# Performance work log

Hardware: AMD Instinct MI355X
Metric: run time of the kernel (lower is better)

## Reference

```python
import jax, jax.numpy as jnp
import numpy as np

B, D, T, BINS = 8, 768, 16384, 1024

def setup_inputs() -> dict:
    key = jax.random.key(0)
    k1, k2, k3, k4 = jax.random.split(key, 4)
    ssl_content = jax.random.normal(k1, (B, D, T), dtype=jnp.float32)
    conv_w = jax.random.normal(k2, (D, D, 2), dtype=jnp.float32) * 0.02  # Conv1d(768,768,k=2,s=2) weight [out,in,k]
    conv_b = jax.random.normal(k3, (D,), dtype=jnp.float32) * 0.02
    codebook = jax.random.normal(k4, (BINS, D), dtype=jnp.float32)
    return {"ssl_content": ssl_content, "conv_w": conv_w, "conv_b": conv_b, "codebook": codebook}

def reference(ssl_content, conv_w, conv_b, codebook):
    # ssl_proj: Conv1d(D, D, kernel_size=2, stride=2), no padding
    ssl = jax.lax.conv_general_dilated(
        ssl_content, conv_w, window_strides=(2,), padding='VALID',
        dimension_numbers=('NCH', 'OIH', 'NCH')) + conv_b[None, :, None]  # [B, D, T//2]
    x = jnp.transpose(ssl, (0, 2, 1))            # b d n -> b n d : [B, T', D]
    b, tq, d = x.shape
    flat = x.reshape(-1, d)                      # [B*T', D]
    # Euclidean codebook search: argmin_k ||flat - codebook[k]||^2
    d2 = (jnp.sum(flat * flat, axis=-1, keepdims=True)
          - 2.0 * (flat @ codebook.T)
          + jnp.sum(codebook * codebook, axis=-1))  # [B*T', BINS]
    codes = jnp.argmin(d2, axis=-1).reshape(b, tq)  # n_q=1 -> indices for quantizer 0: [B, T']
    prompt = codes[0][None, :]                   # codes[0,0].unsqueeze(0) -> [1, T']
    return prompt
```

## Files before the change

### kernel.cpp

```cpp
#include <hip/hip_runtime.h>

#define D    768
#define T    16384
#define TQ   8192
#define BINS 1024
#define K1   1536
#define NKA  (K1 / 32)
#define NKS  (D / 32)
#define FRAG 1024

#define NFRAG_W  ((D / 16) * NKA)
#define NFRAG_CB ((BINS / 16) * NKS)
#define NB_PACKB ((NFRAG_W + NFRAG_CB) / 4)
#define NB_PACKA (NKA * (TQ / 128))
#define NB_CNORM (BINS / 4)

typedef _Float16 f16;
typedef _Float16 h8 __attribute__((ext_vector_type(8)));
typedef float    f32x4 __attribute__((ext_vector_type(4)));


__device__ __forceinline__ void gl_lds16(const void* g, void* l) {
    __builtin_amdgcn_global_load_lds(
        (const __attribute__((address_space(1))) void*)g,
        (__attribute__((address_space(3))) void*)l, 16, 0, 0);
}

__global__ __launch_bounds__(256) void prep_kernel(
    const float* __restrict__ ssl, const float* __restrict__ W,
    const float* __restrict__ cb,
    f16* __restrict__ Whi, f16* __restrict__ Wlo,
    f16* __restrict__ CBhi, f16* __restrict__ CBlo,
    f16* __restrict__ Ahi, f16* __restrict__ Alo,
    float* __restrict__ cnorm)
{
    int b = blockIdx.x;
    int wid = threadIdx.x >> 6, lane = threadIdx.x & 63;

    if (b < NB_PACKB) {
        int fid = b * 4 + wid;
        const float* src; f16* hi; f16* lo; int K, nk, fidl;
        if (fid < NFRAG_W) { src = W;  hi = Whi;  lo = Wlo;  K = K1; nk = NKA; fidl = fid; }
        else               { src = cb; hi = CBhi; lo = CBlo; K = D;  nk = NKS; fidl = fid - NFRAG_W; }
        int r16 = fidl / nk, kblk = fidl - r16 * nk;
        int row = r16 * 16 + (lane & 15);
        int k0  = kblk * 32 + 8 * (lane >> 4);
        const float* s = src + (size_t)row * K + k0;
        float4 v0 = *(const float4*)s;
        float4 v1 = *(const float4*)(s + 4);
        float vv[8] = {v0.x, v0.y, v0.z, v0.w, v1.x, v1.y, v1.z, v1.w};
        h8 vh, vl;
        #pragma unroll
        for (int j = 0; j < 8; ++j) {
            f16 h = (f16)vv[j];
            vh[j] = h;
            vl[j] = (f16)((vv[j] - (float)h) * 2048.f);
        }
        size_t off = ((size_t)fidl * 64 + lane) * 8;
        *(h8*)&hi[off] = vh;
        *(h8*)&lo[off] = vl;
    } else if (b < NB_PACKB + NB_PACKA) {
        int idx = b - NB_PACKB;
        int kblk = idx % NKA, yb = idx / NKA;
        int l15 = lane & 15, lk = lane >> 4;
        #pragma unroll
        for (int q = 0; q < 2; ++q) {
            int tblk = yb * 8 + wid * 2 + q;
            int tp = tblk * 16 + l15;
            int i0 = kblk * 16 + 4 * lk;
            float vv[8];
            #pragma unroll
            for (int ii = 0; ii < 4; ++ii) {
                float2 v = *(const float2*)&ssl[(size_t)(i0 + ii) * T + 2 * tp];
                vv[2 * ii]     = v.x;
                vv[2 * ii + 1] = v.y;
            }
            h8 vh, vl;
            #pragma unroll
            for (int j = 0; j < 8; ++j) {
                f16 h = (f16)vv[j];
                vh[j] = h;
                vl[j] = (f16)((vv[j] - (float)h) * 2048.f);
            }
            size_t off = ((size_t)(tblk * NKA + kblk) * 64 + lane) * 8;
            *(h8*)&Ahi[off] = vh;
            *(h8*)&Alo[off] = vl;
        }
    } else {
        int bin = (b - NB_PACKB - NB_PACKA) * 4 + wid;
        const float* row = cb + (size_t)bin * D;
        float s = 0.f;
        for (int k = lane; k < D; k += 64) { float v = row[k]; s += v * v; }
        #pragma unroll
        for (int off = 32; off > 0; off >>= 1) s += __shfl_down(s, off);
        if (lane == 0) cnorm[bin] = s;
    }
}

__global__ __launch_bounds__(256, 2) void conv_mfma_kernel(
    const f16* __restrict__ Ah, const f16* __restrict__ Al,
    const f16* __restrict__ Bh, const f16* __restrict__ Bl,
    const float* __restrict__ bias,
    f16* __restrict__ Xhi, f16* __restrict__ Xlo)
{
    __shared__ __align__(16) char smem[65536];
    int tid = threadIdx.x, lane = tid & 63, wid = tid >> 6;
    int wm = wid >> 1, wn = wid & 1;
    int l15 = lane & 15, lk = lane >> 4;

    int orig = blockIdx.y * 6 + blockIdx.x;
    int swz  = (orig & 7) * 48 + (orig >> 3);
    int bx = swz % 6, by = swz / 6;

    int mb = by * 128, nb = bx * 128;
    int mb16 = mb >> 4, nb16 = nb >> 4;

    const f16* gsrc; int blk16;
    if      (wid == 0) { gsrc = Ah; blk16 = mb16; }
    else if (wid == 1) { gsrc = Al; blk16 = mb16; }
    else if (wid == 2) { gsrc = Bh; blk16 = nb16; }
    else               { gsrc = Bl; blk16 = nb16; }
    const char* gw = (const char*)gsrc + (size_t)blk16 * NKA * FRAG + lane * 16;
    char* lw0 = smem + wid * 8192;
    char* lw1 = smem + 32768 + wid * 8192;

    const f32x4 zero4 = {0.f, 0.f, 0.f, 0.f};
    f32x4 acc[4][4], acc2[4][4];
    #pragma unroll
    for (int i = 0; i < 4; ++i)
        #pragma unroll
        for (int j = 0; j < 4; ++j) { acc[i][j] = zero4; acc2[i][j] = zero4; }

    #pragma unroll
    for (int f = 0; f < 8; ++f)
        gl_lds16(gw + (size_t)(f * NKA) * FRAG, lw0 + f * FRAG);
    __syncthreads();

    int cur = 0;
    for (int kblk = 0; kblk < NKA; ++kblk) {
        if (kblk + 1 < NKA) {
            char* lwn = cur ? lw0 : lw1;
            #pragma unroll
            for (int f = 0; f < 8; ++f)
                gl_lds16(gw + (size_t)(f * NKA + kblk + 1) * FRAG, lwn + f * FRAG);
        }
        const char* base = smem + cur * 32768;
        h8 ah[4], al[4];
        #pragma unroll
        for (int mf = 0; mf < 4; ++mf) {
            int fo = (wm * 4 + mf) * FRAG + lane * 16;
            ah[mf] = *(const h8*)(base + fo);
            al[mf] = *(const h8*)(base + 8192 + fo);
        }
        #pragma unroll
        for (int nf = 0; nf < 4; ++nf) {
            int fo = (wn * 4 + nf) * FRAG + lane * 16;
            h8 bh = *(const h8*)(base + 16384 + fo);
            h8 bl = *(const h8*)(base + 24576 + fo);
            #pragma unroll
            for (int mf = 0; mf < 4; ++mf) {
                acc [mf][nf] = __builtin_amdgcn_mfma_f32_16x16x32_f16(ah[mf], bh, acc [mf][nf], 0, 0, 0);
                acc2[mf][nf] = __builtin_amdgcn_mfma_f32_16x16x32_f16(ah[mf], bl, acc2[mf][nf], 0, 0, 0);
                acc2[mf][nf] = __builtin_amdgcn_mfma_f32_16x16x32_f16(al[mf], bh, acc2[mf][nf], 0, 0, 0);
            }
        }
        __syncthreads();
        cur ^= 1;
    }

    float* sb = (float*)smem;
    float bv[4];
    #pragma unroll
    for (int nf = 0; nf < 4; ++nf) bv[nf] = bias[nb + wn * 64 + nf * 16 + l15];
    #pragma unroll
    for (int s = 0; s < 4; ++s) {
        __syncthreads();
        if (wm == (s >> 1)) {
            #pragma unroll
            for (int mh = 0; mh < 2; ++mh) {
                int mf = (s & 1) * 2 + mh;
                int srow = mh * 16 + lk * 4;
                #pragma unroll
                for (int nf = 0; nf < 4; ++nf) {
                    int scol = wn * 64 + nf * 16 + l15;
                    #pragma unroll
                    for (int r = 0; r < 4; ++r)
                        sb[(srow + r) * 132 + scol] =
                            acc[mf][nf][r] + acc2[mf][nf][r] * 4.8828125e-4f + bv[nf];
                }
            }
        }
        __syncthreads();
        #pragma unroll
        for (int h = 0; h < 2; ++h) {
            int f = wid * 2 + h;
            int tl = f & 1, dbl = f >> 1;
            int srow = tl * 16 + l15;
            int sd   = dbl * 32 + 8 * lk;
            float vv[8];
            #pragma unroll
            for (int j = 0; j < 8; ++j) vv[j] = sb[srow * 132 + sd + j];
            h8 vh, vl;
            #pragma unroll
            for (int j = 0; j < 8; ++j) {
                f16 hh = (f16)vv[j];
                vh[j] = hh;
                vl[j] = (f16)((vv[j] - (float)hh) * 2048.f);
            }
            int tblk_g = mb16 + s * 2 + tl;
            int dblk_g = (nb >> 5) + dbl;
            size_t off = ((size_t)(tblk_g * NKS + dblk_g) * 64 + lane) * 8;
            *(h8*)&Xhi[off] = vh;
            *(h8*)&Xlo[off] = vl;
        }
    }
}

__global__ __launch_bounds__(256, 2) void score_mfma_kernel(
    const f16* __restrict__ Ah, const f16* __restrict__ Al,
    const f16* __restrict__ Bh, const f16* __restrict__ Bl,
    const float* __restrict__ cnorm,
    float* __restrict__ pval, int* __restrict__ pidx)
{
    __shared__ __align__(16) char smem[65536];
    int tid = threadIdx.x, lane = tid & 63, wid = tid >> 6;
    int wm = wid >> 1, wn = wid & 1;
    int l15 = lane & 15, lk = lane >> 4;

    int orig = blockIdx.y * 8 + blockIdx.x;
    int swz  = (orig & 7) * 64 + (orig >> 3);
    int bx = swz & 7, by = swz >> 3;

    int mb = by * 128, nb = bx * 128;
    int mb16 = mb >> 4, nb16 = nb >> 4;

    const f16* gsrc; int blk16;
    if      (wid == 0) { gsrc = Ah; blk16 = mb16; }
    else if (wid == 1) { gsrc = Al; blk16 = mb16; }
    else if (wid == 2) { gsrc = Bh; blk16 = nb16; }
    else               { gsrc = Bl; blk16 = nb16; }
    const char* gw = (const char*)gsrc + (size_t)blk16 * NKS * FRAG + lane * 16;
    char* lw0 = smem + wid * 8192;
    char* lw1 = smem + 32768 + wid * 8192;

    const f32x4 zero4 = {0.f, 0.f, 0.f, 0.f};
    f32x4 acc[4][4], acc2[4][4];
    #pragma unroll
    for (int i = 0; i < 4; ++i)
        #pragma unroll
        for (int j = 0; j < 4; ++j) { acc[i][j] = zero4; acc2[i][j] = zero4; }

    #pragma unroll
    for (int f = 0; f < 8; ++f)
        gl_lds16(gw + (size_t)(f * NKS) * FRAG, lw0 + f * FRAG);
    __syncthreads();

    int cur = 0;
    for (int kblk = 0; kblk < NKS; ++kblk) {
        if (kblk + 1 < NKS) {
            char* lwn = cur ? lw0 : lw1;
            #pragma unroll
            for (int f = 0; f < 8; ++f)
                gl_lds16(gw + (size_t)(f * NKS + kblk + 1) * FRAG, lwn + f * FRAG);
        }
        const char* base = smem + cur * 32768;
        h8 ah[4], al[4];
        #pragma unroll
        for (int mf = 0; mf < 4; ++mf) {
            int fo = (wm * 4 + mf) * FRAG + lane * 16;
            ah[mf] = *(const h8*)(base + fo);
            al[mf] = *(const h8*)(base + 8192 + fo);
        }
        #pragma unroll
        for (int nf = 0; nf < 4; ++nf) {
            int fo = (wn * 4 + nf) * FRAG + lane * 16;
            h8 bh = *(const h8*)(base + 16384 + fo);
            h8 bl = *(const h8*)(base + 24576 + fo);
            #pragma unroll
            for (int mf = 0; mf < 4; ++mf) {
                acc [mf][nf] = __builtin_amdgcn_mfma_f32_16x16x32_f16(ah[mf], bh, acc [mf][nf], 0, 0, 0);
                acc2[mf][nf] = __builtin_amdgcn_mfma_f32_16x16x32_f16(ah[mf], bl, acc2[mf][nf], 0, 0, 0);
                acc2[mf][nf] = __builtin_amdgcn_mfma_f32_16x16x32_f16(al[mf], bh, acc2[mf][nf], 0, 0, 0);
            }
        }
        __syncthreads();
        cur ^= 1;
    }
    float cn[4];
    #pragma unroll
    for (int nf = 0; nf < 4; ++nf) cn[nf] = cnorm[nb + wn * 64 + nf * 16 + l15];
    int slice = bx * 2 + wn;
    #pragma unroll
    for (int mf = 0; mf < 4; ++mf) {
        #pragma unroll
        for (int r = 0; r < 4; ++r) {
            float v = 3.4e38f; int ix = 0;
            #pragma unroll
            for (int nf = 0; nf < 4; ++nf) {
                float dot = acc[mf][nf][r] + acc2[mf][nf][r] * 4.8828125e-4f;
                float sc = cn[nf] - 2.f * dot;
                int col = nb + wn * 64 + nf * 16 + l15;
                if (sc < v) { v = sc; ix = col; }
            }
            #pragma unroll
            for (int off = 8; off > 0; off >>= 1) {
                float ov = __shfl_xor(v, off);
                int   oi = __shfl_xor(ix, off);
                if (ov < v || (ov == v && oi < ix)) { v = ov; ix = oi; }
            }
            if (l15 == 0) {
                int row = mb + wm * 64 + mf * 16 + lk * 4 + r;
                pval[row * 16 + slice] = v;
                pidx[row * 16 + slice] = ix;
            }
        }
    }
}

__global__ __launch_bounds__(256) void argmin_final_kernel(
    const float* __restrict__ pval, const int* __restrict__ pidx,
    int* __restrict__ out)
{
    int r = blockIdx.x * 256 + threadIdx.x;
    float best = 3.4e38f; int bi = 0;
    #pragma unroll
    for (int s = 0; s < 16; ++s) {
        float v = pval[r * 16 + s];
        if (v < best) { best = v; bi = pidx[r * 16 + s]; }
    }
    out[r] = bi;
}

extern "C" void kernel_launch(void* const* d_in, const int* in_sizes, int n_in,
                              void* d_out, int out_size, void* d_ws, size_t ws_size,
                              hipStream_t stream) {
    const float* ssl = (const float*)d_in[0];
    const float* W   = (const float*)d_in[1];
    const float* bia = (const float*)d_in[2];
    const float* cb  = (const float*)d_in[3];
    int* out = (int*)d_out;

    char* p = (char*)d_ws;
    float* cnorm = (float*)p;  p += 4096;
    f16* Whi  = (f16*)p;  p += (size_t)D * K1 * 2;
    f16* Wlo  = (f16*)p;  p += (size_t)D * K1 * 2;
    f16* CBhi = (f16*)p;  p += (size_t)BINS * D * 2;
    f16* CBlo = (f16*)p;  p += (size_t)BINS * D * 2;
    f16* Ahi  = (f16*)p;  p += (size_t)TQ * K1 * 2;
    f16* Alo  = (f16*)p;  p += (size_t)TQ * K1 * 2;
    f16* Xhi  = (f16*)p;  p += (size_t)TQ * D * 2;
    f16* Xlo  = (f16*)p;  p += (size_t)TQ * D * 2;
    float* pval = (float*)p;  p += (size_t)TQ * 16 * 4;
    int*   pidx = (int*)p;    p += (size_t)TQ * 16 * 4;

    prep_kernel<<<NB_PACKB + NB_PACKA + NB_CNORM, 256, 0, stream>>>(
        ssl, W, cb, Whi, Wlo, CBhi, CBlo, Ahi, Alo, cnorm);
    conv_mfma_kernel<<<dim3(D / 128, TQ / 128), 256, 0, stream>>>(
        Ahi, Alo, Whi, Wlo, bia, Xhi, Xlo);
    score_mfma_kernel<<<dim3(BINS / 128, TQ / 128), 256, 0, stream>>>(
        Xhi, Xlo, CBhi, CBlo, cnorm, pval, pidx);
    argmin_final_kernel<<<TQ / 256, 256, 0, stream>>>(pval, pidx, out);
}
```

Before: 553.2 us.

## Load A fragments directly into registers and stage only B through LDS

Both GEMM kernels now read the A operand (hi/lo fp16 fragments) straight from global memory into registers, double-buffered in registers. Only the B operand is staged through LDS, with all four waves sharing the staging of its 16 fragments. This halves the shared-memory footprint and removes LDS round trips for A, and the k-loop is unrolled by two with explicit ping-pong buffers. In exchange it uses more registers, and each wave does uncached-in-LDS global reads of A that are duplicated across the two wn waves.

```diff
diff --git a/kernel.cpp b/kernel.cpp
--- a/kernel.cpp
+++ b/kernel.cpp
@@ -97,13 +97,53 @@
     }
 }
 
+#define STAGE_B(BH, BL, bufbase, NK, kb)                                      \
+    {                                                                         \
+        _Pragma("unroll")                                                     \
+        for (int j = 0; j < 4; ++j) {                                         \
+            int fg = wid * 4 + j;                                             \
+            const char* gp = (fg < 8 ? (const char*)(BH) : (const char*)(BL)) \
+                + (((size_t)(nb16 + (fg & 7)) * (NK) + (kb)) << 10)           \
+                + lane * 16;                                                  \
+            gl_lds16(gp, (bufbase) + fg * 1024);                              \
+        }                                                                     \
+    }
+
+#define LOAD_A(AHP, ALP, AH, AL, NK, kb)                                      \
+    {                                                                         \
+        _Pragma("unroll")                                                     \
+        for (int mf = 0; mf < 4; ++mf) {                                      \
+            size_t fo = (((size_t)(mb16 + wm * 4 + mf) * (NK) + (kb)) << 10)  \
+                + lane * 16;                                                  \
+            AH[mf] = *(const h8*)((const char*)(AHP) + fo);                   \
+            AL[mf] = *(const h8*)((const char*)(ALP) + fo);                   \
+        }                                                                     \
+    }
+
+#define GEMM_COMPUTE(bufbase, AH, AL)                                         \
+    {                                                                         \
+        const char* bb = (bufbase);                                           \
+        _Pragma("unroll")                                                     \
+        for (int nf = 0; nf < 4; ++nf) {                                      \
+            int fo = (wn * 4 + nf) * 1024 + lane * 16;                        \
+            h8 bh = *(const h8*)(bb + fo);                                    \
+            h8 bl = *(const h8*)(bb + 8192 + fo);                             \
+            _Pragma("unroll")                                                 \
+            for (int mf = 0; mf < 4; ++mf) {                                  \
+                acc [mf][nf] = __builtin_amdgcn_mfma_f32_16x16x32_f16(AH[mf], bh, acc [mf][nf], 0, 0, 0); \
+                acc2[mf][nf] = __builtin_amdgcn_mfma_f32_16x16x32_f16(AH[mf], bl, acc2[mf][nf], 0, 0, 0); \
+                acc2[mf][nf] = __builtin_amdgcn_mfma_f32_16x16x32_f16(AL[mf], bh, acc2[mf][nf], 0, 0, 0); \
+            }                                                                 \
+        }                                                                     \
+    }
+
 __global__ __launch_bounds__(256, 2) void conv_mfma_kernel(
     const f16* __restrict__ Ah, const f16* __restrict__ Al,
     const f16* __restrict__ Bh, const f16* __restrict__ Bl,
     const float* __restrict__ bias,
     f16* __restrict__ Xhi, f16* __restrict__ Xlo)
 {
-    __shared__ __align__(16) char smem[65536];
+    __shared__ __align__(16) char smem[32768];
     int tid = threadIdx.x, lane = tid & 63, wid = tid >> 6;
     int wm = wid >> 1, wn = wid & 1;
     int l15 = lane & 15, lk = lane >> 4;
@@ -111,19 +151,9 @@
     int orig = blockIdx.y * 6 + blockIdx.x;
     int swz  = (orig & 7) * 48 + (orig >> 3);
     int bx = swz % 6, by = swz / 6;
-
     int mb = by * 128, nb = bx * 128;
     int mb16 = mb >> 4, nb16 = nb >> 4;
 
-    const f16* gsrc; int blk16;
-    if      (wid == 0) { gsrc = Ah; blk16 = mb16; }
-    else if (wid == 1) { gsrc = Al; blk16 = mb16; }
-    else if (wid == 2) { gsrc = Bh; blk16 = nb16; }
-    else               { gsrc = Bl; blk16 = nb16; }
-    const char* gw = (const char*)gsrc + (size_t)blk16 * NKA * FRAG + lane * 16;
-    char* lw0 = smem + wid * 8192;
-    char* lw1 = smem + 32768 + wid * 8192;
-
     const f32x4 zero4 = {0.f, 0.f, 0.f, 0.f};
     f32x4 acc[4][4], acc2[4][4];
     #pragma unroll
@@ -131,41 +161,22 @@
         #pragma unroll
         for (int j = 0; j < 4; ++j) { acc[i][j] = zero4; acc2[i][j] = zero4; }
 
-    #pragma unroll
-    for (int f = 0; f < 8; ++f)
-        gl_lds16(gw + (size_t)(f * NKA) * FRAG, lw0 + f * FRAG);
+    h8 a0h[4], a0l[4], a1h[4], a1l[4];
+    LOAD_A(Ah, Al, a0h, a0l, NKA, 0);
+    STAGE_B(Bh, Bl, smem, NKA, 0);
     __syncthreads();
 
-    int cur = 0;
-    for (int kblk = 0; kblk < NKA; ++kblk) {
-        if (kblk + 1 < NKA) {
-            char* lwn = cur ? lw0 : lw1;
-            #pragma unroll
-            for (int f = 0; f < 8; ++f)
-                gl_lds16(gw + (size_t)(f * NKA + kblk + 1) * FRAG, lwn + f * FRAG);
-        }
-        const char* base = smem + cur * 32768;
-        h8 ah[4], al[4];
-        #pragma unroll
-        for (int mf = 0; mf < 4; ++mf) {
-            int fo = (wm * 4 + mf) * FRAG + lane * 16;
-            ah[mf] = *(const h8*)(base + fo);
-            al[mf] = *(const h8*)(base + 8192 + fo);
-        }
-        #pragma unroll
-        for (int nf = 0; nf < 4; ++nf) {
-            int fo = (wn * 4 + nf) * FRAG + lane * 16;
-            h8 bh = *(const h8*)(base + 16384 + fo);
-            h8 bl = *(const h8*)(base + 24576 + fo);
-            #pragma unroll
-            for (int mf = 0; mf < 4; ++mf) {
-                acc [mf][nf] = __builtin_amdgcn_mfma_f32_16x16x32_f16(ah[mf], bh, acc [mf][nf], 0, 0, 0);
-                acc2[mf][nf] = __builtin_amdgcn_mfma_f32_16x16x32_f16(ah[mf], bl, acc2[mf][nf], 0, 0, 0);
-                acc2[mf][nf] = __builtin_amdgcn_mfma_f32_16x16x32_f16(al[mf], bh, acc2[mf][nf], 0, 0, 0);
-            }
-        }
-        __syncthreads();
-        cur ^= 1;
+    for (int kb = 0; kb < NKA; kb += 2) {
+        STAGE_B(Bh, Bl, smem + 16384, NKA, kb + 1);
+        LOAD_A(Ah, Al, a1h, a1l, NKA, kb + 1);
+        GEMM_COMPUTE(smem, a0h, a0l);
+        __syncthreads();
+        if (kb + 2 < NKA) {
+            STAGE_B(Bh, Bl, smem, NKA, kb + 2);
+            LOAD_A(Ah, Al, a0h, a0l, NKA, kb + 2);
+        }
+        GEMM_COMPUTE(smem + 16384, a1h, a1l);
+        __syncthreads();
     }
 
     float* sb = (float*)smem;
@@ -222,7 +233,7 @@
     const float* __restrict__ cnorm,
     float* __restrict__ pval, int* __restrict__ pidx)
 {
-    __shared__ __align__(16) char smem[65536];
+    __shared__ __align__(16) char smem[32768];
     int tid = threadIdx.x, lane = tid & 63, wid = tid >> 6;
     int wm = wid >> 1, wn = wid & 1;
     int l15 = lane & 15, lk = lane >> 4;
@@ -230,19 +241,9 @@
     int orig = blockIdx.y * 8 + blockIdx.x;
     int swz  = (orig & 7) * 64 + (orig >> 3);
     int bx = swz & 7, by = swz >> 3;
-
     int mb = by * 128, nb = bx * 128;
     int mb16 = mb >> 4, nb16 = nb >> 4;
 
-    const f16* gsrc; int blk16;
-    if      (wid == 0) { gsrc = Ah; blk16 = mb16; }
-    else if (wid == 1) { gsrc = Al; blk16 = mb16; }
-    else if (wid == 2) { gsrc = Bh; blk16 = nb16; }
-    else               { gsrc = Bl; blk16 = nb16; }
-    const char* gw = (const char*)gsrc + (size_t)blk16 * NKS * FRAG + lane * 16;
-    char* lw0 = smem + wid * 8192;
-    char* lw1 = smem + 32768 + wid * 8192;
-
     const f32x4 zero4 = {0.f, 0.f, 0.f, 0.f};
     f32x4 acc[4][4], acc2[4][4];
     #pragma unroll
@@ -250,42 +251,24 @@
         #pragma unroll
         for (int j = 0; j < 4; ++j) { acc[i][j] = zero4; acc2[i][j] = zero4; }
 
-    #pragma unroll
-    for (int f = 0; f < 8; ++f)
-        gl_lds16(gw + (size_t)(f * NKS) * FRAG, lw0 + f * FRAG);
+    h8 a0h[4], a0l[4], a1h[4], a1l[4];
+    LOAD_A(Ah, Al, a0h, a0l, NKS, 0);
+    STAGE_B(Bh, Bl, smem, NKS, 0);
     __syncthreads();
 
-    int cur = 0;
-    for (int kblk = 0; kblk < NKS; ++kblk) {
-        if (kblk + 1 < NKS) {
-            char* lwn = cur ? lw0 : lw1;
-            #pragma unroll
-            for (int f = 0; f < 8; ++f)
-                gl_lds16(gw + (size_t)(f * NKS + kblk + 1) * FRAG, lwn + f * FRAG);
-        }
-        const char* base = smem + cur * 32768;
-        h8 ah[4], al[4];
-        #pragma unroll
-        for (int mf = 0; mf < 4; ++mf) {
-            int fo = (wm * 4 + mf) * FRAG + lane * 16;
-            ah[mf] = *(const h8*)(base + fo);
-            al[mf] = *(const h8*)(base + 8192 + fo);
-        }
-        #pragma unroll
-        for (int nf = 0; nf < 4; ++nf) {
-            int fo = (wn * 4 + nf) * FRAG + lane * 16;
-            h8 bh = *(const h8*)(base + 16384 + fo);
-            h8 bl = *(const h8*)(base + 24576 + fo);
-            #pragma unroll
-            for (int mf = 0; mf < 4; ++mf) {
-                acc [mf][nf] = __builtin_amdgcn_mfma_f32_16x16x32_f16(ah[mf], bh, acc [mf][nf], 0, 0, 0);
-                acc2[mf][nf] = __builtin_amdgcn_mfma_f32_16x16x32_f16(ah[mf], bl, acc2[mf][nf], 0, 0, 0);
-                acc2[mf][nf] = __builtin_amdgcn_mfma_f32_16x16x32_f16(al[mf], bh, acc2[mf][nf], 0, 0, 0);
-            }
-        }
-        __syncthreads();
-        cur ^= 1;
-    }
+    for (int kb = 0; kb < NKS; kb += 2) {
+        STAGE_B(Bh, Bl, smem + 16384, NKS, kb + 1);
+        LOAD_A(Ah, Al, a1h, a1l, NKS, kb + 1);
+        GEMM_COMPUTE(smem, a0h, a0l);
+        __syncthreads();
+        if (kb + 2 < NKS) {
+            STAGE_B(Bh, Bl, smem, NKS, kb + 2);
+            LOAD_A(Ah, Al, a0h, a0l, NKS, kb + 2);
+        }
+        GEMM_COMPUTE(smem + 16384, a1h, a1l);
+        __syncthreads();
+    }
+
     float cn[4];
     #pragma unroll
     for (int nf = 0; nf < 4; ++nf) cn[nf] = cnorm[nb + wn * 64 + nf * 16 + l15];
```

New measurement: 559.5 us. Within noise of the previous version (+1.1%).
